# Kernel tuning notes

Hardware: AMD Instinct MI355X
Metric: run time of the kernel (lower is better)

Reference implementation:

```python
import jax, jax.numpy as jnp
import numpy as np


def setup_inputs() -> dict:
    key = jax.random.key(0)
    k1, _ = jax.random.split(key)
    x = jax.random.normal(k1, (2, 16, 16, 16, 64), dtype=jnp.float32)
    gamma = jnp.ones((1,), dtype=jnp.float32)  # learned scalar (zeros at init; ones to make output nontrivial)
    return {"x": x, "gamma": gamma}


def reference(x, gamma):
    # x: (B, D, H, W, C); faithful to the Keras layer: flatten spatial dims,
    # energy = Q @ Q^T over the N=D*H*W axis, softmax(axis=-1), attn @ Q,
    # then gamma-scaled residual add.
    B, D, H, W, C = x.shape
    N = D * H * W
    q = x.reshape(B, N, C)                            # proj_query (B, N, C)
    energy = jnp.einsum('bnc,bmc->bnm', q, q)          # (B, N, N)
    attn = jax.nn.softmax(energy, axis=-1)
    out = jnp.einsum('bnm,bmc->bnc', attn, q)          # (B, N, C)
    out = out.reshape(B, D, H, W, C)
    return gamma * out + x
```

## Files before the change

### kernel.cpp

```cpp
#include <hip/hip_runtime.h>
#include <hip/hip_bf16.h>
#include <math.h>


#define NN 4096
#define CC 64
#define LOG2E 1.4426950408889634f

typedef __attribute__((ext_vector_type(4))) float f32x4;
typedef __attribute__((ext_vector_type(8))) short bf16x8;
typedef __attribute__((ext_vector_type(4))) short bf16x4;
typedef unsigned short u16;
typedef __attribute__((ext_vector_type(4))) u16 u16x4;
typedef __attribute__((ext_vector_type(2))) unsigned u32x2;

__device__ inline u16 f2bf(float f) {
  union { float f; unsigned u; } v; v.f = f;
  unsigned r = (v.u + 0x7fffu + ((v.u >> 16) & 1u)) >> 16;
  return (u16)r;
}
__device__ inline float bf2f(short h) {
  union { unsigned u; float f; } v;
  v.u = ((unsigned)(unsigned short)h) << 16;
  return v.f;
}
__device__ inline unsigned fbits(float f) {
  union { float f; unsigned u; } v; v.f = f;
  return v.u;
}
__device__ inline bf16x8 cvt8(f32x4 a, f32x4 b) {
  bf16x8 r;
  r[0] = (short)f2bf(a[0]); r[1] = (short)f2bf(a[1]);
  r[2] = (short)f2bf(a[2]); r[3] = (short)f2bf(a[3]);
  r[4] = (short)f2bf(b[0]); r[5] = (short)f2bf(b[1]);
  r[6] = (short)f2bf(b[2]); r[7] = (short)f2bf(b[3]);
  return r;
}

__global__ __launch_bounds__(256) void prep_kernel(const float* __restrict__ x,
                                                   u16* __restrict__ Qb,
                                                   u16* __restrict__ Vt) {
  __shared__ u16 t[64][20];
  int b = blockIdx.x >> 8;
  int n0 = (blockIdx.x & 255) << 4;
  const f32x4* x4 = (const f32x4*)(x + ((size_t)b * NN + n0) * CC);
  u16* qb = Qb + ((size_t)b * NN + n0) * CC;
  {
    int idx4 = threadIdx.x;
    int i = idx4 >> 4, cg = idx4 & 15;
    f32x4 v = x4[idx4];
    u16x4 h;
    h[0] = f2bf(v[0]); h[1] = f2bf(v[1]); h[2] = f2bf(v[2]); h[3] = f2bf(v[3]);
    *(u16x4*)(qb + (size_t)i * CC + cg * 4) = h;
    t[cg * 4 + 0][i] = h[0]; t[cg * 4 + 1][i] = h[1];
    t[cg * 4 + 2][i] = h[2]; t[cg * 4 + 3][i] = h[3];
  }
  __syncthreads();
  int kb = n0 >> 6, kw0 = n0 & 63;
  {
    int idx4 = threadIdx.x;
    int c = idx4 >> 2, i4 = (idx4 & 3) * 4;
    u16x4 h = *(const u16x4*)(&t[c][i4]);
    *(u16x4*)(Vt + (((size_t)b * (NN / 64) + kb) * 64 + c) * 64 + kw0 + i4) = h;
  }
}

template <int S>
__global__ __launch_bounds__(128, 2) void attn_split(
    const u16* __restrict__ Qb, const u16* __restrict__ Vt,
    u16* __restrict__ Opart, float* __restrict__ lpart) {
  constexpr int KPS = NN / S;
  constexpr int ITERS = KPS / 64;
  const int w = threadIdx.x >> 6;
  const int lane = threadIdx.x & 63;
  const int quad = lane >> 4, col = lane & 15;
  const int blk = blockIdx.x;
  const int b = blk / (64 * S);
  const int rb = (blk / S) & 63;
  const int s = blk % S;

  __shared__ u16 KT[2][64 * 64];
  __shared__ u16 VT[2][64 * 64];
  __shared__ u16 PB[2][16 * 72];

  const u16* Qbase = Qb + (size_t)b * NN * CC;
  const u16* Vbase = Vt + (size_t)b * NN * CC;
  const int row0 = rb * 64 + w * 32;

  bf16x8 qs0[2], qs1[2];
  float m_sc[2];
#pragma unroll
  for (int rt = 0; rt < 2; ++rt) {
    const u16* qp = Qbase + (size_t)(row0 + rt * 16 + col) * CC + quad * 8;
    bf16x8 r0 = *(const bf16x8*)qp;
    bf16x8 r1 = *(const bf16x8*)(qp + 32);
    float msum = 0.f;
#pragma unroll
    for (int j = 0; j < 8; ++j) {
      float a0 = bf2f(r0[j]), a1 = bf2f(r1[j]);
      u16 h0 = f2bf(a0 * LOG2E), h1 = f2bf(a1 * LOG2E);
      qs0[rt][j] = (short)h0; qs1[rt][j] = (short)h1;
      msum += bf2f((short)h0) * a0 + bf2f((short)h1) * a1;
    }
    msum += __shfl_xor(msum, 16);
    msum += __shfl_xor(msum, 32);
    m_sc[rt] = msum;
  }

  f32x4 zero = {0.f, 0.f, 0.f, 0.f};
  f32x4 acc[2][4] = {{zero, zero, zero, zero}, {zero, zero, zero, zero}};
  float l_loc[2] = {0.f, 0.f};

  const int kk = lane >> 3;
  const int sw = (lane & 7) ^ kk;
  const u16* kptr = Qbase + (size_t)(s * KPS + w * 32 + kk) * CC + sw * 8;
  const u16* vptr = Vbase + ((size_t)(s * KPS >> 6) * 64 + (w * 32 + kk)) * 64 + sw * 8;

#define STAGE(p, kp, vp)                                                      \
  {                                                                           \
    _Pragma("unroll")                                                         \
    for (int g = 0; g < 4; ++g) {                                             \
      __builtin_amdgcn_global_load_lds(                                       \
          (const __attribute__((address_space(1))) unsigned*)((kp) + g * 512),\
          (__attribute__((address_space(3))) unsigned*)&KT[p][(w * 32 + g * 8) * 64], \
          16, 0, 0);                                                          \
      __builtin_amdgcn_global_load_lds(                                       \
          (const __attribute__((address_space(1))) unsigned*)((vp) + g * 512),\
          (__attribute__((address_space(3))) unsigned*)&VT[p][(w * 32 + g * 8) * 64], \
          16, 0, 0);                                                          \
    }                                                                         \
  }

  STAGE(0, kptr, vptr)
#pragma unroll 2
  for (int i = 0; i < ITERS; ++i) {
    __syncthreads();
    const int p = i & 1;
    if (i + 1 < ITERS) STAGE(p ^ 1, kptr + 4096, vptr + 4096)
    kptr += 4096; vptr += 4096;

    const int cs = col & 7;
    bf16x8 ka[4], kb_[4], va[4], vb[4];
#pragma unroll
    for (int t = 0; t < 4; ++t) {
      ka[t]  = *(const bf16x8*)&KT[p][(t * 16 + col) * 64 + (quad ^ cs) * 8];
      kb_[t] = *(const bf16x8*)&KT[p][(t * 16 + col) * 64 + ((quad + 4) ^ cs) * 8];
      va[t]  = *(const bf16x8*)&VT[p][(t * 16 + col) * 64 + (quad ^ cs) * 8];
      vb[t]  = *(const bf16x8*)&VT[p][(t * 16 + col) * 64 + ((quad + 4) ^ cs) * 8];
    }
#pragma unroll
    for (int rt = 0; rt < 2; ++rt) {
      f32x4 sx[4];
#pragma unroll
      for (int t = 0; t < 4; ++t) {
        sx[t] = __builtin_amdgcn_mfma_f32_16x16x32_bf16(ka[t], qs0[rt], zero, 0, 0, 0);
        sx[t] = __builtin_amdgcn_mfma_f32_16x16x32_bf16(kb_[t], qs1[rt], sx[t], 0, 0, 0);
      }
      u16* PBw = &PB[w][0];
#pragma unroll
      for (int t = 0; t < 4; ++t) {
        f32x4 pv;
#pragma unroll
        for (int r = 0; r < 4; ++r) pv[r] = exp2f(sx[t][r] - m_sc[rt]);
        l_loc[rt] += pv[0] + pv[1] + pv[2] + pv[3];
        u32x2 d;
        d[0] = __builtin_amdgcn_perm(fbits(pv[1]), fbits(pv[0]), 0x07060302u);
        d[1] = __builtin_amdgcn_perm(fbits(pv[3]), fbits(pv[2]), 0x07060302u);
        *(u32x2*)&PBw[col * 72 + t * 16 + quad * 4] = d;
      }
      bf16x8 pf0 = *(const bf16x8*)&PBw[col * 72 + quad * 8];
      bf16x8 pf1 = *(const bf16x8*)&PBw[col * 72 + 32 + quad * 8];
#pragma unroll
      for (int cg = 0; cg < 4; ++cg) {
        acc[rt][cg] = __builtin_amdgcn_mfma_f32_16x16x32_bf16(pf0, va[cg], acc[rt][cg], 0, 0, 0);
        acc[rt][cg] = __builtin_amdgcn_mfma_f32_16x16x32_bf16(pf1, vb[cg], acc[rt][cg], 0, 0, 0);
      }
    }
  }
#undef STAGE

  size_t pbase = (((size_t)(b * 64 + rb)) * S + s) * (64 * 64);
  size_t lbase = (((size_t)(b * 64 + rb)) * S + s) * 64;
#pragma unroll
  for (int rt = 0; rt < 2; ++rt) {
    float l = l_loc[rt];
    l += __shfl_xor(l, 16);
    l += __shfl_xor(l, 32);
    if (quad == 0) lpart[lbase + w * 32 + rt * 16 + col] = l;
#pragma unroll
    for (int r = 0; r < 4; ++r) {
      int lr = w * 32 + rt * 16 + quad * 4 + r;
      size_t o = pbase + (size_t)lr * 64;
      Opart[o + col]      = f2bf(acc[rt][0][r]);
      Opart[o + col + 16] = f2bf(acc[rt][1][r]);
      Opart[o + col + 32] = f2bf(acc[rt][2][r]);
      Opart[o + col + 48] = f2bf(acc[rt][3][r]);
    }
  }
}

template <int S>
__global__ __launch_bounds__(256) void epi_kernel(
    const float* __restrict__ x, const float* __restrict__ gamma,
    const u16* __restrict__ Opart, const float* __restrict__ lpart,
    float* __restrict__ out) {
  int t = blockIdx.x * 256 + threadIdx.x;
  int cg = t & 15;
  int n = (t >> 4) & (NN - 1);
  int b = t >> 16;
  int rb = n >> 6, lr = n & 63;
  size_t obase = ((size_t)(b * 64 + rb) * S) * 4096 + (size_t)lr * 64 + cg * 4;
  size_t lbase = ((size_t)(b * 64 + rb) * S) * 64 + lr;
  f32x4 sO = {0.f, 0.f, 0.f, 0.f};
  float sL = 0.f;
#pragma unroll
  for (int s = 0; s < S; ++s) {
    u16x4 o4 = *(const u16x4*)(Opart + obase + (size_t)s * 4096);
    sL += lpart[lbase + s * 64];
    sO[0] += bf2f((short)o4[0]); sO[1] += bf2f((short)o4[1]);
    sO[2] += bf2f((short)o4[2]); sO[3] += bf2f((short)o4[3]);
  }
  size_t xi = (((size_t)b * NN + n) * CC + cg * 4);
  f32x4 xv = *(const f32x4*)(x + xi);
  float g = gamma[0], inv = 1.f / sL;
  f32x4 ov;
#pragma unroll
  for (int j = 0; j < 4; ++j) ov[j] = g * (sO[j] * inv) + xv[j];
  *(f32x4*)(((float*)out) + xi) = ov;
}

template <int WPB>
__global__ __launch_bounds__(WPB * 64, 4) void attn_fast(
    const float* __restrict__ x, const float* __restrict__ gamma,
    const u16* __restrict__ Qb, const u16* __restrict__ Vt,
    float* __restrict__ out) {
  const int w = threadIdx.x >> 6;
  const int lane = threadIdx.x & 63;
  const int quad = lane >> 4, col = lane & 15;
  const int b = blockIdx.x >> 8;
  const int tile = (blockIdx.x & 255) << 4;

  extern __shared__ char smem[];
  float* Osh = (float*)smem;
  float* lsh = Osh + WPB * 1024;
  u16* pl = (u16*)(lsh + WPB * 16) + w * 2176;

  const size_t xoff = (size_t)b * NN * CC;
  const u16* Qbase = Qb + xoff;
  const u16* Vbase = Vt + xoff;

  bf16x8 qf0 = *(const bf16x8*)(Qbase + (size_t)(tile + col) * CC + quad * 8);
  bf16x8 qf1 = *(const bf16x8*)(Qbase + (size_t)(tile + col) * CC + 32 + quad * 8);

  float msum = 0.f;
#pragma unroll
  for (int j = 0; j < 8; ++j) {
    float a = bf2f(qf0[j]), c = bf2f(qf1[j]);
    msum += a * a + c * c;
  }
  msum += __shfl_xor(msum, 16);
  msum += __shfl_xor(msum, 32);
  float m_i[4];
#pragma unroll
  for (int r = 0; r < 4; ++r) m_i[r] = __shfl(msum, quad * 4 + r);

  f32x4 zero = {0.f, 0.f, 0.f, 0.f};
  f32x4 acc[4] = {zero, zero, zero, zero};
  float l_i[4] = {0.f, 0.f, 0.f, 0.f};

  const int k0 = w * (NN / WPB);
#pragma unroll 2
  for (int kt = k0; kt < k0 + NN / WPB; kt += 64) {
    u16* plc = pl + ((kt >> 6) & 1) * 1088;
    f32x4 sx[4];
#pragma unroll
    for (int t = 0; t < 4; ++t) {
      const u16* kp = Qbase + (size_t)(kt + t * 16 + col) * CC + quad * 8;
      bf16x8 ka = *(const bf16x8*)kp;
      bf16x8 kb = *(const bf16x8*)(kp + 32);
      sx[t] = __builtin_amdgcn_mfma_f32_16x16x32_bf16(qf0, ka, zero, 0, 0, 0);
      sx[t] = __builtin_amdgcn_mfma_f32_16x16x32_bf16(qf1, kb, sx[t], 0, 0, 0);
    }
#pragma unroll
    for (int t = 0; t < 4; ++t) {
#pragma unroll
      for (int r = 0; r < 4; ++r) {
        float p = __expf(sx[t][r] - m_i[r]);
        l_i[r] += p;
        plc[(quad * 4 + r) * 68 + t * 16 + col] = f2bf(p);
      }
    }
    bf16x8 pf0 = *(const bf16x8*)(plc + col * 68 + quad * 8);
    bf16x8 pf1 = *(const bf16x8*)(plc + col * 68 + 32 + quad * 8);
#pragma unroll
    for (int cg = 0; cg < 4; ++cg) {
      const u16* vp = Vbase + (((size_t)(kt >> 6)) * 64 + cg * 16 + col) * 64 + quad * 8;
      bf16x8 v0 = *(const bf16x8*)vp;
      bf16x8 v1 = *(const bf16x8*)(vp + 32);
      acc[cg] = __builtin_amdgcn_mfma_f32_16x16x32_bf16(pf0, v0, acc[cg], 0, 0, 0);
      acc[cg] = __builtin_amdgcn_mfma_f32_16x16x32_bf16(pf1, v1, acc[cg], 0, 0, 0);
    }
  }

#pragma unroll
  for (int r = 0; r < 4; ++r)
#pragma unroll
    for (int off = 1; off < 16; off <<= 1) l_i[r] += __shfl_xor(l_i[r], off, 16);
#pragma unroll
  for (int r = 0; r < 4; ++r) {
    int row = quad * 4 + r;
    Osh[(w * 16 + row) * 64 + col]      = acc[0][r];
    Osh[(w * 16 + row) * 64 + col + 16] = acc[1][r];
    Osh[(w * 16 + row) * 64 + col + 32] = acc[2][r];
    Osh[(w * 16 + row) * 64 + col + 48] = acc[3][r];
    if (col == 0) lsh[w * 16 + row] = l_i[r];
  }
  __syncthreads();

  float g = gamma[0];
  for (int row = w; row < 16; row += WPB) {
    float L = 0.f, val = 0.f;
#pragma unroll
    for (int w2 = 0; w2 < WPB; ++w2) {
      L += lsh[w2 * 16 + row];
      val += Osh[(w2 * 16 + row) * 64 + lane];
    }
    size_t o = xoff + (size_t)(tile + row) * CC + lane;
    out[o] = g * (val / L) + x[o];
  }
}

template <int WPB>
__global__ __launch_bounds__(512) void attn_fb(const float* __restrict__ x,
                                               const float* __restrict__ gamma,
                                               float* __restrict__ out) {
  const int w = threadIdx.x >> 6;
  const int lane = threadIdx.x & 63;
  const int quad = lane >> 4, col = lane & 15;
  const int b = blockIdx.x >> 8;
  const int tile = (blockIdx.x & 255) << 4;

  extern __shared__ char smem[];
  float* Osh = (float*)smem;
  float* msh = Osh + WPB * 1024;
  float* lsh = msh + WPB * 16;
  u16* pl = (u16*)(lsh + WPB * 16) + w * 768;
  u16* vt = (u16*)(lsh + WPB * 16) + WPB * 768 + w * 2176;

  const size_t xoff = (size_t)b * NN * CC;
  const f32x4* x4 = (const f32x4*)(x + xoff);

  bf16x8 qf0, qf1;
  {
    int ri = (tile + col) * 16 + quad * 2;
    qf0 = cvt8(x4[ri], x4[ri + 1]);
    qf1 = cvt8(x4[ri + 8], x4[ri + 9]);
  }
  f32x4 zero = {0.f, 0.f, 0.f, 0.f};
  f32x4 acc0 = zero, acc1 = zero, acc2 = zero, acc3 = zero;
  float m_i[4], l_i[4];
#pragma unroll
  for (int r = 0; r < 4; ++r) { m_i[r] = -1e30f; l_i[r] = 0.f; }

  const int k0 = w * (NN / WPB);
  for (int kt = k0; kt < k0 + NN / WPB; kt += 32) {
    bf16x8 k00, k01, k10, k11;
    {
      int kb = (kt + col) * 16 + quad * 2;
      k00 = cvt8(x4[kb], x4[kb + 1]);
      k01 = cvt8(x4[kb + 8], x4[kb + 9]);
      k10 = cvt8(x4[kb + 256], x4[kb + 257]);
      k11 = cvt8(x4[kb + 264], x4[kb + 265]);
#pragma unroll
      for (int h = 0; h < 2; ++h) {
        bf16x8 va = h ? k10 : k00, vb = h ? k11 : k01;
        int base = (h * 16 + col) * 68 + quad * 8;
        *(bf16x4*)(vt + base) = __builtin_shufflevector(va, va, 0, 1, 2, 3);
        *(bf16x4*)(vt + base + 4) = __builtin_shufflevector(va, va, 4, 5, 6, 7);
        *(bf16x4*)(vt + base + 32) = __builtin_shufflevector(vb, vb, 0, 1, 2, 3);
        *(bf16x4*)(vt + base + 36) = __builtin_shufflevector(vb, vb, 4, 5, 6, 7);
      }
    }
    f32x4 s0 = zero, s1 = zero;
    s0 = __builtin_amdgcn_mfma_f32_16x16x32_bf16(qf0, k00, s0, 0, 0, 0);
    s0 = __builtin_amdgcn_mfma_f32_16x16x32_bf16(qf1, k01, s0, 0, 0, 0);
    s1 = __builtin_amdgcn_mfma_f32_16x16x32_bf16(qf0, k10, s1, 0, 0, 0);
    s1 = __builtin_amdgcn_mfma_f32_16x16x32_bf16(qf1, k11, s1, 0, 0, 0);

    float p0[4], p1[4], alpha[4];
#pragma unroll
    for (int r = 0; r < 4; ++r) {
      float mx = fmaxf(s0[r], s1[r]);
#pragma unroll
      for (int off = 1; off < 16; off <<= 1) mx = fmaxf(mx, __shfl_xor(mx, off, 16));
      float mn = fmaxf(m_i[r], mx);
      alpha[r] = __expf(m_i[r] - mn);
      p0[r] = __expf(s0[r] - mn);
      p1[r] = __expf(s1[r] - mn);
      float rs = p0[r] + p1[r];
#pragma unroll
      for (int off = 1; off < 16; off <<= 1) rs += __shfl_xor(rs, off, 16);
      l_i[r] = l_i[r] * alpha[r] + rs;
      m_i[r] = mn;
    }
#pragma unroll
    for (int r = 0; r < 4; ++r) {
      acc0[r] *= alpha[r]; acc1[r] *= alpha[r];
      acc2[r] *= alpha[r]; acc3[r] *= alpha[r];
    }
#pragma unroll
    for (int r = 0; r < 4; ++r) {
      pl[(quad * 4 + r) * 24 + col] = f2bf(p0[r]);
      pl[384 + (quad * 4 + r) * 24 + col] = f2bf(p1[r]);
    }
    bf16x8 pf = *(const bf16x8*)(pl + (quad >> 1) * 384 + col * 24 + (quad & 1) * 8);

    bf16x8 v0, v1, v2, v3;
#pragma unroll
    for (int j = 0; j < 8; ++j) {
      int rb = (quad * 8 + j) * 68 + col;
      v0[j] = (short)vt[rb];
      v1[j] = (short)vt[rb + 16];
      v2[j] = (short)vt[rb + 32];
      v3[j] = (short)vt[rb + 48];
    }
    acc0 = __builtin_amdgcn_mfma_f32_16x16x32_bf16(pf, v0, acc0, 0, 0, 0);
    acc1 = __builtin_amdgcn_mfma_f32_16x16x32_bf16(pf, v1, acc1, 0, 0, 0);
    acc2 = __builtin_amdgcn_mfma_f32_16x16x32_bf16(pf, v2, acc2, 0, 0, 0);
    acc3 = __builtin_amdgcn_mfma_f32_16x16x32_bf16(pf, v3, acc3, 0, 0, 0);
  }

#pragma unroll
  for (int r = 0; r < 4; ++r) {
    int row = quad * 4 + r;
    Osh[(w * 16 + row) * 64 + col] = acc0[r];
    Osh[(w * 16 + row) * 64 + col + 16] = acc1[r];
    Osh[(w * 16 + row) * 64 + col + 32] = acc2[r];
    Osh[(w * 16 + row) * 64 + col + 48] = acc3[r];
    if (col == 0) { msh[w * 16 + row] = m_i[r]; lsh[w * 16 + row] = l_i[r]; }
  }
  __syncthreads();

  float g = gamma[0];
  for (int row = w; row < 16; row += WPB) {
    float M = -1e30f;
#pragma unroll
    for (int w2 = 0; w2 < WPB; ++w2) M = fmaxf(M, msh[w2 * 16 + row]);
    float L = 0.f, val = 0.f;
#pragma unroll
    for (int w2 = 0; w2 < WPB; ++w2) {
      float e = __expf(msh[w2 * 16 + row] - M);
      L += lsh[w2 * 16 + row] * e;
      val += Osh[(w2 * 16 + row) * 64 + lane] * e;
    }
    size_t o = xoff + (size_t)(tile + row) * CC + lane;
    out[o] = g * (val / L) + x[o];
  }
}

extern "C" void kernel_launch(void* const* d_in, const int* in_sizes, int n_in,
                              void* d_out, int out_size, void* d_ws, size_t ws_size,
                              hipStream_t stream) {
  const float* x = (const float*)d_in[0];
  const float* gamma = (const float*)d_in[1];
  float* out = (float*)d_out;

  constexpr int S = 8;
  constexpr size_t kQV = (size_t)2 * 2 * NN * CC * sizeof(u16);
  constexpr size_t kOp = (size_t)2 * 64 * S * 64 * 64 * sizeof(u16);
  constexpr size_t kLp = (size_t)2 * 64 * S * 64 * sizeof(float);
  if (ws_size >= kQV + kOp + kLp) {
    u16* Qb = (u16*)d_ws;
    u16* Vt = Qb + (size_t)2 * NN * CC;
    u16* Opart = (u16*)((char*)d_ws + kQV);
    float* lpart = (float*)((char*)d_ws + kQV + kOp);
    prep_kernel<<<512, 256, 0, stream>>>(x, Qb, Vt);
    attn_split<S><<<2 * 64 * S, 128, 0, stream>>>(Qb, Vt, Opart, lpart);
    epi_kernel<S><<<(2 * NN * 16) / 256, 256, 0, stream>>>(x, gamma, Opart, lpart, out);
  } else if (ws_size >= kQV) {
    u16* Qb = (u16*)d_ws;
    u16* Vt = Qb + (size_t)2 * NN * CC;
    prep_kernel<<<512, 256, 0, stream>>>(x, Qb, Vt);
    constexpr int SM = 8 * 1024 * 4 + 8 * 16 * 4 + 8 * 2176 * 2;
    attn_fast<8><<<512, 512, SM, stream>>>(x, gamma, Qb, Vt, out);
  } else {
    constexpr int SM4 = 4 * (1024 + 32) * 4 + 4 * 768 * 2 + 4 * 2176 * 2;
    attn_fb<4><<<512, 256, SM4, stream>>>(x, gamma, out);
  }
}
```

Measured before the change: 83.28 us.

## Split attention block across four waves with 16 query rows each

The split-K attention kernel now runs 256 threads (4 waves) per block, with each wave owning 16 query rows instead of 32. The per-iteration K/V tile loads into LDS are shared across four waves, and each wave stages half as many rows. K and V fragments are read from LDS just before use instead of being held in registers, which cuts register pressure so that four blocks per CU can be resident. The P buffer layout changes from padded to XOR-swizzled. The intent is more waves to hide latency and lower VGPR use. In exchange, each wave performs more LDS reads per MFMA and there are more waves hitting each barrier.

```diff
diff --git a/kernel.cpp b/kernel.cpp
--- a/kernel.cpp
+++ b/kernel.cpp
@@ -66,7 +66,7 @@
 }
 
 template <int S>
-__global__ __launch_bounds__(128, 2) void attn_split(
+__global__ __launch_bounds__(256, 4) void attn_split(
     const u16* __restrict__ Qb, const u16* __restrict__ Vt,
     u16* __restrict__ Opart, float* __restrict__ lpart) {
   constexpr int KPS = NN / S;
@@ -76,22 +76,21 @@
   const int quad = lane >> 4, col = lane & 15;
   const int blk = blockIdx.x;
   const int b = blk / (64 * S);
-  const int rb = (blk / S) & 63;
+  const int rg = (blk / S) & 63;
   const int s = blk % S;
 
   __shared__ u16 KT[2][64 * 64];
   __shared__ u16 VT[2][64 * 64];
-  __shared__ u16 PB[2][16 * 72];
+  __shared__ u16 PB[4][16 * 64];
 
   const u16* Qbase = Qb + (size_t)b * NN * CC;
   const u16* Vbase = Vt + (size_t)b * NN * CC;
-  const int row0 = rb * 64 + w * 32;
-
-  bf16x8 qs0[2], qs1[2];
-  float m_sc[2];
-#pragma unroll
-  for (int rt = 0; rt < 2; ++rt) {
-    const u16* qp = Qbase + (size_t)(row0 + rt * 16 + col) * CC + quad * 8;
+  const int row0 = rg * 64 + w * 16;
+
+  bf16x8 qs0, qs1;
+  float m_sc;
+  {
+    const u16* qp = Qbase + (size_t)(row0 + col) * CC + quad * 8;
     bf16x8 r0 = *(const bf16x8*)qp;
     bf16x8 r1 = *(const bf16x8*)(qp + 32);
     float msum = 0.f;
@@ -99,39 +98,41 @@
     for (int j = 0; j < 8; ++j) {
       float a0 = bf2f(r0[j]), a1 = bf2f(r1[j]);
       u16 h0 = f2bf(a0 * LOG2E), h1 = f2bf(a1 * LOG2E);
-      qs0[rt][j] = (short)h0; qs1[rt][j] = (short)h1;
+      qs0[j] = (short)h0; qs1[j] = (short)h1;
       msum += bf2f((short)h0) * a0 + bf2f((short)h1) * a1;
     }
     msum += __shfl_xor(msum, 16);
     msum += __shfl_xor(msum, 32);
-    m_sc[rt] = msum;
+    m_sc = msum;
   }
 
   f32x4 zero = {0.f, 0.f, 0.f, 0.f};
-  f32x4 acc[2][4] = {{zero, zero, zero, zero}, {zero, zero, zero, zero}};
-  float l_loc[2] = {0.f, 0.f};
+  f32x4 acc[4] = {zero, zero, zero, zero};
+  float l_loc = 0.f;
 
   const int kk = lane >> 3;
   const int sw = (lane & 7) ^ kk;
-  const u16* kptr = Qbase + (size_t)(s * KPS + w * 32 + kk) * CC + sw * 8;
-  const u16* vptr = Vbase + ((size_t)(s * KPS >> 6) * 64 + (w * 32 + kk)) * 64 + sw * 8;
+  const u16* kptr = Qbase + (size_t)(s * KPS + w * 16 + kk) * CC + sw * 8;
+  const u16* vptr = Vbase + ((size_t)(s * KPS >> 6) * 64 + (w * 16 + kk)) * 64 + sw * 8;
 
 #define STAGE(p, kp, vp)                                                      \
   {                                                                           \
     _Pragma("unroll")                                                         \
-    for (int g = 0; g < 4; ++g) {                                             \
+    for (int g = 0; g < 2; ++g) {                                             \
       __builtin_amdgcn_global_load_lds(                                       \
           (const __attribute__((address_space(1))) unsigned*)((kp) + g * 512),\
-          (__attribute__((address_space(3))) unsigned*)&KT[p][(w * 32 + g * 8) * 64], \
+          (__attribute__((address_space(3))) unsigned*)&KT[p][(w * 16 + g * 8) * 64], \
           16, 0, 0);                                                          \
       __builtin_amdgcn_global_load_lds(                                       \
           (const __attribute__((address_space(1))) unsigned*)((vp) + g * 512),\
-          (__attribute__((address_space(3))) unsigned*)&VT[p][(w * 32 + g * 8) * 64], \
+          (__attribute__((address_space(3))) unsigned*)&VT[p][(w * 16 + g * 8) * 64], \
           16, 0, 0);                                                          \
     }                                                                         \
   }
 
   STAGE(0, kptr, vptr)
+  const int cs = col & 7;
+  u16* PBw = &PB[w][0];
 #pragma unroll 2
   for (int i = 0; i < ITERS; ++i) {
     __syncthreads();
@@ -139,63 +140,53 @@
     if (i + 1 < ITERS) STAGE(p ^ 1, kptr + 4096, vptr + 4096)
     kptr += 4096; vptr += 4096;
 
-    const int cs = col & 7;
-    bf16x8 ka[4], kb_[4], va[4], vb[4];
+    f32x4 sx[4];
 #pragma unroll
     for (int t = 0; t < 4; ++t) {
-      ka[t]  = *(const bf16x8*)&KT[p][(t * 16 + col) * 64 + (quad ^ cs) * 8];
-      kb_[t] = *(const bf16x8*)&KT[p][(t * 16 + col) * 64 + ((quad + 4) ^ cs) * 8];
-      va[t]  = *(const bf16x8*)&VT[p][(t * 16 + col) * 64 + (quad ^ cs) * 8];
-      vb[t]  = *(const bf16x8*)&VT[p][(t * 16 + col) * 64 + ((quad + 4) ^ cs) * 8];
-    }
-#pragma unroll
-    for (int rt = 0; rt < 2; ++rt) {
-      f32x4 sx[4];
-#pragma unroll
-      for (int t = 0; t < 4; ++t) {
-        sx[t] = __builtin_amdgcn_mfma_f32_16x16x32_bf16(ka[t], qs0[rt], zero, 0, 0, 0);
-        sx[t] = __builtin_amdgcn_mfma_f32_16x16x32_bf16(kb_[t], qs1[rt], sx[t], 0, 0, 0);
-      }
-      u16* PBw = &PB[w][0];
-#pragma unroll
-      for (int t = 0; t < 4; ++t) {
-        f32x4 pv;
-#pragma unroll
-        for (int r = 0; r < 4; ++r) pv[r] = exp2f(sx[t][r] - m_sc[rt]);
-        l_loc[rt] += pv[0] + pv[1] + pv[2] + pv[3];
-        u32x2 d;
-        d[0] = __builtin_amdgcn_perm(fbits(pv[1]), fbits(pv[0]), 0x07060302u);
-        d[1] = __builtin_amdgcn_perm(fbits(pv[3]), fbits(pv[2]), 0x07060302u);
-        *(u32x2*)&PBw[col * 72 + t * 16 + quad * 4] = d;
-      }
-      bf16x8 pf0 = *(const bf16x8*)&PBw[col * 72 + quad * 8];
-      bf16x8 pf1 = *(const bf16x8*)&PBw[col * 72 + 32 + quad * 8];
-#pragma unroll
-      for (int cg = 0; cg < 4; ++cg) {
-        acc[rt][cg] = __builtin_amdgcn_mfma_f32_16x16x32_bf16(pf0, va[cg], acc[rt][cg], 0, 0, 0);
-        acc[rt][cg] = __builtin_amdgcn_mfma_f32_16x16x32_bf16(pf1, vb[cg], acc[rt][cg], 0, 0, 0);
-      }
+      bf16x8 ka = *(const bf16x8*)&KT[p][(t * 16 + col) * 64 + (quad ^ cs) * 8];
+      bf16x8 kb = *(const bf16x8*)&KT[p][(t * 16 + col) * 64 + ((quad + 4) ^ cs) * 8];
+      sx[t] = __builtin_amdgcn_mfma_f32_16x16x32_bf16(ka, qs0, zero, 0, 0, 0);
+      sx[t] = __builtin_amdgcn_mfma_f32_16x16x32_bf16(kb, qs1, sx[t], 0, 0, 0);
+    }
+#pragma unroll
+    for (int t = 0; t < 4; ++t) {
+      f32x4 pv;
+#pragma unroll
+      for (int r = 0; r < 4; ++r) pv[r] = exp2f(sx[t][r] - m_sc);
+      l_loc += pv[0] + pv[1] + pv[2] + pv[3];
+      u32x2 d;
+      d[0] = __builtin_amdgcn_perm(fbits(pv[1]), fbits(pv[0]), 0x07060302u);
+      d[1] = __builtin_amdgcn_perm(fbits(pv[3]), fbits(pv[2]), 0x07060302u);
+      *(u32x2*)&PBw[col * 64 + ((t * 2 + (quad >> 1)) ^ cs) * 8 + (quad & 1) * 4] = d;
+    }
+    bf16x8 pf0 = *(const bf16x8*)&PBw[col * 64 + (quad ^ cs) * 8];
+    bf16x8 pf1 = *(const bf16x8*)&PBw[col * 64 + ((quad + 4) ^ cs) * 8];
+#pragma unroll
+    for (int cg = 0; cg < 4; ++cg) {
+      bf16x8 va = *(const bf16x8*)&VT[p][(cg * 16 + col) * 64 + (quad ^ cs) * 8];
+      bf16x8 vb = *(const bf16x8*)&VT[p][(cg * 16 + col) * 64 + ((quad + 4) ^ cs) * 8];
+      acc[cg] = __builtin_amdgcn_mfma_f32_16x16x32_bf16(pf0, va, acc[cg], 0, 0, 0);
+      acc[cg] = __builtin_amdgcn_mfma_f32_16x16x32_bf16(pf1, vb, acc[cg], 0, 0, 0);
     }
   }
 #undef STAGE
 
-  size_t pbase = (((size_t)(b * 64 + rb)) * S + s) * (64 * 64);
-  size_t lbase = (((size_t)(b * 64 + rb)) * S + s) * 64;
-#pragma unroll
-  for (int rt = 0; rt < 2; ++rt) {
-    float l = l_loc[rt];
+  size_t pbase = (((size_t)(b * 64 + rg)) * S + s) * (64 * 64);
+  size_t lbase = (((size_t)(b * 64 + rg)) * S + s) * 64;
+  {
+    float l = l_loc;
     l += __shfl_xor(l, 16);
     l += __shfl_xor(l, 32);
-    if (quad == 0) lpart[lbase + w * 32 + rt * 16 + col] = l;
-#pragma unroll
-    for (int r = 0; r < 4; ++r) {
-      int lr = w * 32 + rt * 16 + quad * 4 + r;
-      size_t o = pbase + (size_t)lr * 64;
-      Opart[o + col]      = f2bf(acc[rt][0][r]);
-      Opart[o + col + 16] = f2bf(acc[rt][1][r]);
-      Opart[o + col + 32] = f2bf(acc[rt][2][r]);
-      Opart[o + col + 48] = f2bf(acc[rt][3][r]);
-    }
+    if (quad == 0) lpart[lbase + w * 16 + col] = l;
+  }
+#pragma unroll
+  for (int r = 0; r < 4; ++r) {
+    int lr = w * 16 + quad * 4 + r;
+    size_t o = pbase + (size_t)lr * 64;
+    Opart[o + col]      = f2bf(acc[0][r]);
+    Opart[o + col + 16] = f2bf(acc[1][r]);
+    Opart[o + col + 32] = f2bf(acc[2][r]);
+    Opart[o + col + 48] = f2bf(acc[3][r]);
   }
 }
 
@@ -475,7 +466,7 @@
     u16* Opart = (u16*)((char*)d_ws + kQV);
     float* lpart = (float*)((char*)d_ws + kQV + kOp);
     prep_kernel<<<512, 256, 0, stream>>>(x, Qb, Vt);
-    attn_split<S><<<2 * 64 * S, 128, 0, stream>>>(Qb, Vt, Opart, lpart);
+    attn_split<S><<<2 * 64 * S, 256, 0, stream>>>(Qb, Vt, Opart, lpart);
     epi_kernel<S><<<(2 * NN * 16) / 256, 256, 0, stream>>>(x, gamma, Opart, lpart, out);
   } else if (ws_size >= kQV) {
     u16* Qb = (u16*)d_ws;
```

Result: no change. 81.75 us, median of 2 (-1.8%).
